# Performance work log

Measured on AMD Instinct MI355X. Metric: run time of the kernel, lower is better.

Reference implementation:

```python
import jax, jax.numpy as jnp
import numpy as np

B, S = 2, 2048
DIM, NH = 2048, 16
QLR, KVLR = 768, 512
NOPE, ROPE, VDIM = 128, 64, 128
IH, IHD, ITOPK = 16, 128, 512
NEG = -1e9


def _rope_half(x, cos, sin):
    # non-interleaved rotary (pairs (x_i, x_{i+d/2})); x: [b,s,h,d], cos/sin: [s,d//2]
    d2 = x.shape[-1] // 2
    x1, x2 = x[..., :d2], x[..., d2:]
    c = cos[None, :, None, :]
    s = sin[None, :, None, :]
    return jnp.concatenate([x1 * c - x2 * s, x1 * s + x2 * c], axis=-1)


def _rmsnorm(x, w, eps=1e-6):
    var = jnp.mean(x * x, axis=-1, keepdims=True)
    return w * x * jax.lax.rsqrt(var + eps)


def _layernorm(x, w, b, eps=1e-6):
    m = jnp.mean(x, axis=-1, keepdims=True)
    v = jnp.mean((x - m) ** 2, axis=-1, keepdims=True)
    return (x - m) * jax.lax.rsqrt(v + eps) * w + b


def setup_inputs() -> dict:
    key = jax.random.key(0)
    ks = jax.random.split(key, 10)

    def w(k, shape):
        return jax.random.normal(k, shape, jnp.float32) * 0.02

    x = jax.random.normal(ks[0], (B, S, DIM), jnp.float32)
    inv_freq = 1.0 / (10000.0 ** (jnp.arange(0, ROPE, 2, dtype=jnp.float32) / ROPE))
    ang = jnp.arange(S, dtype=jnp.float32)[:, None] * inv_freq[None, :]  # [S, ROPE//2]
    causal = jnp.triu(jnp.ones((S, S), dtype=bool), k=1)
    mask = jnp.where(causal, NEG, 0.0).astype(jnp.float32)
    return {
        "x": x,
        "freqs_cos": jnp.cos(ang),
        "freqs_sin": jnp.sin(ang),
        "mask": mask,
        "wq_a": w(ks[1], (QLR, DIM)),
        "q_norm_w": jnp.ones((QLR,), jnp.float32),
        "wq_b": w(ks[2], (NH * (NOPE + ROPE), QLR)),
        "wkv_a": w(ks[3], (KVLR + ROPE, DIM)),
        "kv_norm_w": jnp.ones((KVLR,), jnp.float32),
        "wkv_b": w(ks[4], (NH * (NOPE + VDIM), KVLR)),
        "wo": w(ks[5], (DIM, NH * VDIM)),
        "idx_wq_b": w(ks[6], (IH * IHD, QLR)),
        "idx_wk": w(ks[7], (IHD, DIM)),
        "idx_k_norm_w": jnp.ones((IHD,), jnp.float32),
        "idx_k_norm_b": jnp.zeros((IHD,), jnp.float32),
        "idx_weights_proj": w(ks[8], (IH, DIM)),
        "start_pos": 0,
    }


def _indexer(x, qr, freqs_cos, freqs_sin, mask,
             idx_wq_b, idx_wk, idx_k_norm_w, idx_k_norm_b, idx_weights_proj):
    b, s, _ = x.shape
    q = (qr @ idx_wq_b.T).reshape(b, s, IH, IHD)
    q_pe, q_nope = q[..., :ROPE], q[..., ROPE:]  # rope part FIRST in indexer
    q = jnp.concatenate([_rope_half(q_pe, freqs_cos, freqs_sin), q_nope], axis=-1)
    k = _layernorm(x @ idx_wk.T, idx_k_norm_w, idx_k_norm_b)  # [b,s,IHD]
    k_pe, k_nope = k[..., :ROPE], k[..., ROPE:]
    k_pe = _rope_half(k_pe[:, :, None, :], freqs_cos, freqs_sin)[:, :, 0, :]
    k = jnp.concatenate([k_pe, k_nope], axis=-1)
    # weights_proj(x) * n_heads**-0.5 * softmax_scale(= head_dim**-0.5)
    weights = (x @ idx_weights_proj.T) * (IH ** -0.5) * (IHD ** -0.5)  # [b,s,IH]
    logits = jax.nn.relu(jnp.einsum('bshd,btd->bsth', q, k))
    index_score = jnp.einsum('bsth,bsh->bst', logits, weights) + mask[None]
    _, topk = jax.lax.top_k(index_score, ITOPK)
    return topk  # [b,s,ITOPK] int32


def reference(x, freqs_cos, freqs_sin, mask, wq_a, q_norm_w, wq_b, wkv_a, kv_norm_w,
              wkv_b, wo, idx_wq_b, idx_wk, idx_k_norm_w, idx_k_norm_b,
              idx_weights_proj, start_pos):
    b, s, _ = x.shape
    qr = _rmsnorm(x @ wq_a.T, q_norm_w)  # shared low-rank query latent [b,s,QLR]
    q = (qr @ wq_b.T).reshape(b, s, NH, NOPE + ROPE)
    q_nope, q_pe = q[..., :NOPE], q[..., NOPE:]  # nope part first in MLA
    q_pe = _rope_half(q_pe, freqs_cos, freqs_sin)
    kv = x @ wkv_a.T  # [b,s,KVLR+ROPE]
    kv, k_pe = kv[..., :KVLR], kv[..., KVLR:]
    k_pe = _rope_half(k_pe[:, :, None, :], freqs_cos, freqs_sin)[:, :, 0, :]  # [b,t,ROPE]
    kv = _rmsnorm(kv, kv_norm_w)  # latent kv cache (prefill: full sequence) [b,t,KVLR]
    wkv_b3 = wkv_b.reshape(NH, NOPE + VDIM, KVLR)
    # absorb k up-projection into q (weight absorption trick)
    q_abs = jnp.einsum('bshd,hdc->bshc', q_nope, wkv_b3[:, :NOPE])
    scale = (NOPE + ROPE) ** -0.5
    scores = (jnp.einsum('bshc,btc->bsht', q_abs, kv)
              + jnp.einsum('bshr,btr->bsht', q_pe, k_pe)) * scale
    topk = _indexer(x, qr, freqs_cos, freqs_sin, mask,
                    idx_wq_b, idx_wk, idx_k_norm_w, idx_k_norm_b, idx_weights_proj)
    bi = jnp.arange(b)[:, None, None]
    si = jnp.arange(s)[None, :, None]
    sel = jnp.zeros((b, s, s), dtype=bool).at[bi, si, topk].set(True)
    index_mask = jnp.where(sel, 0.0, NEG) + mask[None]  # [b,s,t]
    scores = scores + index_mask[:, :, None, :]
    p = jax.nn.softmax(scores, axis=-1)
    o = jnp.einsum('bsht,btc->bshc', p, kv)
    o = jnp.einsum('bshc,hdc->bshd', o, wkv_b3[:, NOPE:])  # v up-projection
    return o.reshape(b, s, NH * VDIM) @ wo.T
```

## Files before the change

### kernel.cpp

```cpp
#include <hip/hip_runtime.h>

typedef short bf16x8 __attribute__((ext_vector_type(8)));
typedef _Float16 f16x8 __attribute__((ext_vector_type(8)));
typedef float f32x4 __attribute__((ext_vector_type(4)));
typedef _Float16 f16;
typedef unsigned short u16;
typedef unsigned int u32;

#define DEVFN static __device__ __forceinline__

DEVFN u16 f2bf(float f) {
  u32 u = __builtin_bit_cast(u32, f);
  return (u16)((u + 0x7FFFu + ((u >> 16) & 1u)) >> 16);
}

DEVFN void glds16(const void* g, void* l) {
  __builtin_amdgcn_global_load_lds((const __attribute__((address_space(1))) void*)g,
                                   (__attribute__((address_space(3))) void*)l, 16, 0, 0);
}

DEVFN void wsplit(f16* oh, f16* ol, long o, float v) {
  f16 hh = (f16)v;
  oh[o] = hh;
  ol[o] = (f16)((v - (float)hh) * 2048.0f);
}

DEVFN long idxq_off(int row, int h, int c) {
  return ((((long)(row >> 4) * 16 + h) * 4 + (c >> 5)) * 4 + ((c >> 3) & 3)) * 128
         + (long)(row & 15) * 8 + (c & 7);
}

__global__ __launch_bounds__(256) void k_cvt_bf16(const float* __restrict__ in, u16* __restrict__ out, long n) {
  long i = ((long)blockIdx.x * 256 + threadIdx.x) * 4;
  if (i < n) {
    float4 v = *(const float4*)(in + i);
    out[i] = f2bf(v.x); out[i + 1] = f2bf(v.y); out[i + 2] = f2bf(v.z); out[i + 3] = f2bf(v.w);
  }
}

__global__ __launch_bounds__(256) void k_split(const float* __restrict__ in, f16* __restrict__ oh, f16* __restrict__ ol, long n) {
  long i = ((long)blockIdx.x * 256 + threadIdx.x) * 4;
  if (i < n) {
    float4 v = *(const float4*)(in + i);
    float a[4] = {v.x, v.y, v.z, v.w};
    #pragma unroll
    for (int k = 0; k < 4; ++k) {
      f16 hh = (f16)a[k];
      oh[i + k] = hh;
      ol[i + k] = (f16)((a[k] - (float)hh) * 2048.0f);
    }
  }
}

__global__ __launch_bounds__(256) void k_cvt_split_x(const float* __restrict__ in, u16* __restrict__ ob,
    f16* __restrict__ oh, f16* __restrict__ ol, long n) {
  long i = ((long)blockIdx.x * 256 + threadIdx.x) * 4;
  if (i < n) {
    float4 v = *(const float4*)(in + i);
    float a[4] = {v.x, v.y, v.z, v.w};
    #pragma unroll
    for (int k = 0; k < 4; ++k) {
      ob[i + k] = f2bf(a[k]);
      f16 hh = (f16)a[k];
      oh[i + k] = hh;
      ol[i + k] = (f16)((a[k] - (float)hh) * 2048.0f);
    }
  }
}

__global__ __launch_bounds__(256) void k_cvt_wkvb(const float* __restrict__ wkvb, u16* __restrict__ full_b, u16* __restrict__ nope_t) {
  long i = (long)blockIdx.x * 256 + threadIdx.x;
  if (i >= 2097152) return;
  float v = wkvb[i];
  u16 bv = f2bf(v);
  full_b[i] = bv;
  long row = i >> 9;
  int c = (int)(i & 511);
  int h = (int)(row >> 8);
  int d = (int)(row & 255);
  if (d < 128) nope_t[(long)h * 65536 + (long)c * 128 + d] = bv;
}

__global__ __launch_bounds__(256) void k_gemm_bt(
    const u16* __restrict__ A, const u16* __restrict__ B, void* __restrict__ Cout,
    int N, int K, long lda, long ldb, long ldc, long sA, long sB, long sC, int outBf16) {
  A += (long)blockIdx.z * sA;
  B += (long)blockIdx.z * sB;
  const long m0 = (long)blockIdx.y * 128;
  const long n0 = (long)blockIdx.x * 128;
  __shared__ __align__(16) u16 As[128 * 32];
  __shared__ __align__(16) u16 Bs[128 * 32];
  const int tid = threadIdx.x;
  const int lane = tid & 63, wid = tid >> 6;
  const int g = lane >> 4, l16 = lane & 15;
  const int srow = tid >> 2;
  const int scol = (tid & 3) * 8;
  const int wm = wid >> 1, wn = wid & 1;
  f32x4 acc[4][4];
  #pragma unroll
  for (int m = 0; m < 4; ++m)
    #pragma unroll
    for (int n = 0; n < 4; ++n) acc[m][n] = (f32x4){0.f, 0.f, 0.f, 0.f};
  for (int k0 = 0; k0 < K; k0 += 32) {
    long rb0 = n0 + srow; if (rb0 >= N) rb0 = 0;
    long rb1 = n0 + 64 + srow; if (rb1 >= N) rb1 = 0;
    glds16(A + (m0 + srow) * lda + k0 + scol, As + (size_t)wid * 512);
    glds16(A + (m0 + 64 + srow) * lda + k0 + scol, As + 2048 + (size_t)wid * 512);
    glds16(B + rb0 * ldb + k0 + scol, Bs + (size_t)wid * 512);
    glds16(B + rb1 * ldb + k0 + scol, Bs + 2048 + (size_t)wid * 512);
    __syncthreads();
    bf16x8 af[4], bfv[4];
    #pragma unroll
    for (int m = 0; m < 4; ++m) af[m] = *(const bf16x8*)(As + (wm * 64 + m * 16 + l16) * 32 + g * 8);
    #pragma unroll
    for (int n = 0; n < 4; ++n) bfv[n] = *(const bf16x8*)(Bs + (wn * 64 + n * 16 + l16) * 32 + g * 8);
    #pragma unroll
    for (int m = 0; m < 4; ++m)
      #pragma unroll
      for (int n = 0; n < 4; ++n)
        acc[m][n] = __builtin_amdgcn_mfma_f32_16x16x32_bf16(af[m], bfv[n], acc[m][n], 0, 0, 0);
    __syncthreads();
  }
  const long cz = (long)blockIdx.z * sC;
  if (outBf16) {
    u16* C = (u16*)Cout;
    #pragma unroll
    for (int m = 0; m < 4; ++m) {
      const long row = m0 + wm * 64 + m * 16 + g * 4;
      #pragma unroll
      for (int n = 0; n < 4; ++n) {
        const long col = n0 + wn * 64 + n * 16 + l16;
        if (col < N) {
          #pragma unroll
          for (int r = 0; r < 4; ++r) C[cz + (row + r) * ldc + col] = f2bf(acc[m][n][r]);
        }
      }
    }
  } else {
    float* C = (float*)Cout;
    #pragma unroll
    for (int m = 0; m < 4; ++m) {
      const long row = m0 + wm * 64 + m * 16 + g * 4;
      #pragma unroll
      for (int n = 0; n < 4; ++n) {
        const long col = n0 + wn * 64 + n * 16 + l16;
        if (col < N) {
          #pragma unroll
          for (int r = 0; r < 4; ++r) C[cz + (row + r) * ldc + col] = acc[m][n][r];
        }
      }
    }
  }
}

__global__ __launch_bounds__(256) void k_gemm_f16pair(
    const f16* __restrict__ Ah, const f16* __restrict__ Al,
    const f16* __restrict__ Bh, const f16* __restrict__ Bl,
    float* __restrict__ C, int N, int K, long lda, long ldb, long ldc) {
  const long m0 = (long)blockIdx.y * 128;
  const long n0 = (long)blockIdx.x * 128;
  __shared__ __align__(16) f16 AhS[4096], AlS[4096], BhS[4096], BlS[4096];
  const int tid = threadIdx.x;
  const int lane = tid & 63, wid = tid >> 6;
  const int g = lane >> 4, l16 = lane & 15;
  const int srow = tid >> 2;
  const int scol = (tid & 3) * 8;
  const int wm = wid >> 1, wn = wid & 1;
  f32x4 a0[4][4], a1[4][4];
  #pragma unroll
  for (int m = 0; m < 4; ++m)
    #pragma unroll
    for (int n = 0; n < 4; ++n) { a0[m][n] = (f32x4){0.f,0.f,0.f,0.f}; a1[m][n] = (f32x4){0.f,0.f,0.f,0.f}; }
  for (int k0 = 0; k0 < K; k0 += 32) {
    long rb0 = n0 + srow; if (rb0 >= N) rb0 = 0;
    long rb1 = n0 + 64 + srow; if (rb1 >= N) rb1 = 0;
    glds16(Ah + (m0 + srow) * lda + k0 + scol, AhS + (size_t)wid * 512);
    glds16(Ah + (m0 + 64 + srow) * lda + k0 + scol, AhS + 2048 + (size_t)wid * 512);
    glds16(Al + (m0 + srow) * lda + k0 + scol, AlS + (size_t)wid * 512);
    glds16(Al + (m0 + 64 + srow) * lda + k0 + scol, AlS + 2048 + (size_t)wid * 512);
    glds16(Bh + rb0 * ldb + k0 + scol, BhS + (size_t)wid * 512);
    glds16(Bh + rb1 * ldb + k0 + scol, BhS + 2048 + (size_t)wid * 512);
    glds16(Bl + rb0 * ldb + k0 + scol, BlS + (size_t)wid * 512);
    glds16(Bl + rb1 * ldb + k0 + scol, BlS + 2048 + (size_t)wid * 512);
    __syncthreads();
    f16x8 ah[4], al[4];
    #pragma unroll
    for (int m = 0; m < 4; ++m) {
      ah[m] = *(const f16x8*)(AhS + (wm * 64 + m * 16 + l16) * 32 + g * 8);
      al[m] = *(const f16x8*)(AlS + (wm * 64 + m * 16 + l16) * 32 + g * 8);
    }
    #pragma unroll
    for (int n = 0; n < 4; ++n) {
      f16x8 bh = *(const f16x8*)(BhS + (wn * 64 + n * 16 + l16) * 32 + g * 8);
      f16x8 bl = *(const f16x8*)(BlS + (wn * 64 + n * 16 + l16) * 32 + g * 8);
      #pragma unroll
      for (int m = 0; m < 4; ++m) {
        a0[m][n] = __builtin_amdgcn_mfma_f32_16x16x32_f16(ah[m], bh, a0[m][n], 0, 0, 0);
        a1[m][n] = __builtin_amdgcn_mfma_f32_16x16x32_f16(ah[m], bl, a1[m][n], 0, 0, 0);
        a1[m][n] = __builtin_amdgcn_mfma_f32_16x16x32_f16(al[m], bh, a1[m][n], 0, 0, 0);
      }
    }
    __syncthreads();
  }
  #pragma unroll
  for (int m = 0; m < 4; ++m) {
    const long row = m0 + wm * 64 + m * 16 + g * 4;
    #pragma unroll
    for (int n = 0; n < 4; ++n) {
      const long col = n0 + wn * 64 + n * 16 + l16;
      if (col < N) {
        #pragma unroll
        for (int r = 0; r < 4; ++r)
          C[(row + r) * ldc + col] = a0[m][n][r] + a1[m][n][r] * 4.8828125e-4f;
      }
    }
  }
}

__global__ __launch_bounds__(256) void k_rms_qr(float* __restrict__ qr, const float* __restrict__ w,
    f16* __restrict__ qh, f16* __restrict__ ql, u16* __restrict__ qb) {
  const int row = blockIdx.x, tid = threadIdx.x;
  float v[3];
  float ss = 0.f;
  #pragma unroll
  for (int i = 0; i < 3; ++i) { v[i] = qr[(long)row * 768 + tid + i * 256]; ss += v[i] * v[i]; }
  #pragma unroll
  for (int m = 1; m < 64; m <<= 1) ss += __shfl_xor(ss, m, 64);
  __shared__ float wsum[4];
  if ((tid & 63) == 0) wsum[tid >> 6] = ss;
  __syncthreads();
  float tot = wsum[0] + wsum[1] + wsum[2] + wsum[3];
  float gsc = 1.0f / sqrtf(tot * (1.0f / 768.0f) + 1e-6f);
  #pragma unroll
  for (int i = 0; i < 3; ++i) {
    long o = (long)row * 768 + tid + i * 256;
    float y = v[i] * gsc * w[tid + i * 256];
    qr[o] = y;
    f16 hh = (f16)y;
    qh[o] = hh;
    ql[o] = (f16)((y - (float)hh) * 2048.0f);
    qb[o] = f2bf(y);
  }
}

__global__ __launch_bounds__(256) void k_kvpost(const float* __restrict__ kvraw, const float* __restrict__ w,
    const float* __restrict__ cosb, const float* __restrict__ sinb,
    u16* __restrict__ kvc, u16* __restrict__ kpe) {
  const int row = blockIdx.x, tid = threadIdx.x;
  const int s = row & 2047;
  float v0 = kvraw[(long)row * 576 + tid];
  float v1 = kvraw[(long)row * 576 + 256 + tid];
  float ss = v0 * v0 + v1 * v1;
  #pragma unroll
  for (int m = 1; m < 64; m <<= 1) ss += __shfl_xor(ss, m, 64);
  __shared__ float wsum[4];
  if ((tid & 63) == 0) wsum[tid >> 6] = ss;
  __syncthreads();
  float tot = wsum[0] + wsum[1] + wsum[2] + wsum[3];
  float gsc = 1.0f / sqrtf(tot * (1.0f / 512.0f) + 1e-6f);
  kvc[(long)row * 512 + tid] = f2bf(v0 * gsc * w[tid]);
  kvc[(long)row * 512 + 256 + tid] = f2bf(v1 * gsc * w[256 + tid]);
  if (tid < 32) {
    float x1 = kvraw[(long)row * 576 + 512 + tid];
    float x2 = kvraw[(long)row * 576 + 544 + tid];
    float c = cosb[s * 32 + tid], sn = sinb[s * 32 + tid];
    kpe[(long)row * 64 + tid] = f2bf(x1 * c - x2 * sn);
    kpe[(long)row * 64 + 32 + tid] = f2bf(x1 * sn + x2 * c);
  }
}

__global__ __launch_bounds__(256) void k_qpost(const float* __restrict__ q,
    const float* __restrict__ cosb, const float* __restrict__ sinb,
    u16* __restrict__ qn, u16* __restrict__ qpe) {
  const int row = blockIdx.x, tid = threadIdx.x;
  const int s = row & 2047;
  const long qb = (long)row * 3072;
  #pragma unroll
  for (int i = 0; i < 8; ++i) {
    int idx = tid + i * 256;
    int h = idx >> 7, d = idx & 127;
    qn[(long)row * 2048 + idx] = f2bf(q[qb + h * 192 + d]);
  }
  #pragma unroll
  for (int i = 0; i < 2; ++i) {
    int p = tid + i * 256;
    int h = p >> 5, e = p & 31;
    float x1 = q[qb + h * 192 + 128 + e];
    float x2 = q[qb + h * 192 + 160 + e];
    float c = cosb[s * 32 + e], sn = sinb[s * 32 + e];
    qpe[(long)row * 1024 + h * 64 + e] = f2bf(x1 * c - x2 * sn);
    qpe[(long)row * 1024 + h * 64 + 32 + e] = f2bf(x1 * sn + x2 * c);
  }
}

__global__ __launch_bounds__(256) void k_idxqpost(const float* __restrict__ iq,
    const float* __restrict__ cosb, const float* __restrict__ sinb,
    f16* __restrict__ oh, f16* __restrict__ ol) {
  const int row = blockIdx.x, tid = threadIdx.x;
  const int s = row & 2047;
  const long ib = (long)row * 2048;
  #pragma unroll
  for (int i = 0; i < 2; ++i) {
    int p = tid + i * 256;
    int h = p >> 5, e = p & 31;
    float x1 = iq[ib + h * 128 + e], x2 = iq[ib + h * 128 + 32 + e];
    float c = cosb[s * 32 + e], sn = sinb[s * 32 + e];
    wsplit(oh, ol, idxq_off(row, h, e), x1 * c - x2 * sn);
    wsplit(oh, ol, idxq_off(row, h, e + 32), x1 * sn + x2 * c);
  }
  #pragma unroll
  for (int i = 0; i < 4; ++i) {
    int idx = tid + i * 256;
    int h = idx >> 6, e2 = idx & 63;
    int c = 64 + e2;
    wsplit(oh, ol, idxq_off(row, h, c), iq[ib + h * 128 + c]);
  }
}

__global__ __launch_bounds__(128) void k_idxkpost(const float* __restrict__ ik,
    const float* __restrict__ w, const float* __restrict__ bb,
    const float* __restrict__ cosb, const float* __restrict__ sinb,
    f16* __restrict__ oh, f16* __restrict__ ol) {
  const int row = blockIdx.x, tid = threadIdx.x;
  const int s = row & 2047;
  float v = ik[(long)row * 128 + tid];
  float sum = v;
  #pragma unroll
  for (int m = 1; m < 64; m <<= 1) sum += __shfl_xor(sum, m, 64);
  __shared__ float r0[2], r1[2];
  __shared__ float ybuf[128];
  if ((tid & 63) == 0) r0[tid >> 6] = sum;
  __syncthreads();
  float mean = (r0[0] + r0[1]) * (1.0f / 128.0f);
  float d = v - mean;
  float s2 = d * d;
  #pragma unroll
  for (int m = 1; m < 64; m <<= 1) s2 += __shfl_xor(s2, m, 64);
  if ((tid & 63) == 0) r1[tid >> 6] = s2;
  __syncthreads();
  float var = (r1[0] + r1[1]) * (1.0f / 128.0f);
  float y = d * (1.0f / sqrtf(var + 1e-6f)) * w[tid] + bb[tid];
  ybuf[tid] = y;
  __syncthreads();
  float outv = y;
  if (tid < 64) {
    int e = tid & 31;
    float x1 = ybuf[e], x2 = ybuf[32 + e];
    float c = cosb[s * 32 + e], sn = sinb[s * 32 + e];
    outv = (tid < 32) ? (x1 * c - x2 * sn) : (x1 * sn + x2 * c);
  }
  int csw = tid ^ ((row & 7) << 3);
  long o = (long)row * 128 + csw;
  f16 hh = (f16)outv;
  oh[o] = hh;
  ol[o] = (f16)((outv - (float)hh) * 2048.0f);
}

__global__ __launch_bounds__(256) void k_wproj(const float* __restrict__ x,
    const float* __restrict__ proj, float* __restrict__ out) {
  const int row = blockIdx.x, tid = threadIdx.x;
  __shared__ float xr[2048];
  #pragma unroll
  for (int i = 0; i < 8; ++i) xr[tid + i * 256] = x[(long)row * 2048 + tid + i * 256];
  __syncthreads();
  int h = tid >> 4, seg = tid & 15;
  float acc = 0.f;
  for (int k = 0; k < 128; ++k) acc += xr[seg * 128 + k] * proj[h * 2048 + seg * 128 + k];
  #pragma unroll
  for (int m = 1; m < 16; m <<= 1) acc += __shfl_xor(acc, m, 64);
  if (seg == 0) out[(long)row * 16 + h] = acc * 0.25f * 0.08838834764831843f;
}

__global__ __launch_bounds__(256) void k_iscore(
    const f16* __restrict__ Ah, const f16* __restrict__ Al,
    const f16* __restrict__ Bh, const f16* __restrict__ Bl,
    const float* __restrict__ wts, float* __restrict__ out) {
  const int b = blockIdx.z;
  const int s0 = blockIdx.y * 64, t0 = blockIdx.x * 128;
  if (t0 > s0 + 63) return;
  __shared__ __align__(16) f16 BhS[128 * 128];
  __shared__ __align__(16) f16 BlS[128 * 128];
  const int tid = threadIdx.x;
  const int lane = tid & 63, wid = tid >> 6;
  const int g = lane >> 4, l16 = lane & 15;
  const long brow = ((long)b * 2048 + t0) * 128;
  #pragma unroll
  for (int c = 0; c < 8; ++c) {
    int row = c * 16 + (tid >> 4);
    int col = (tid & 15) * 8;
    glds16(Bh + brow + (long)row * 128 + col, BhS + (size_t)c * 2048 + (size_t)wid * 512);
    glds16(Bl + brow + (long)row * 128 + col, BlS + (size_t)c * 2048 + (size_t)wid * 512);
  }
  __syncthreads();
  const int ws_ = wid >> 1, wt = wid & 1;
  f32x4 sc[2][4];
  #pragma unroll
  for (int m = 0; m < 2; ++m)
    #pragma unroll
    for (int n = 0; n < 4; ++n) sc[m][n] = (f32x4){0.f, 0.f, 0.f, 0.f};
  for (int h = 0; h < 16; ++h) {
    f16x8 ah[2][4], al[2][4];
    #pragma unroll
    for (int m = 0; m < 2; ++m) {
      int rt = (b * 2048 + s0 + ws_ * 32 + m * 16) >> 4;
      #pragma unroll
      for (int kc = 0; kc < 4; ++kc) {
        long o = ((((long)rt * 16 + h) * 4 + kc) * 4 + g) * 128 + l16 * 8;
        ah[m][kc] = *(const f16x8*)(Ah + o);
        al[m][kc] = *(const f16x8*)(Al + o);
      }
    }
    f32x4 l0[2][4], l1[2][4];
    #pragma unroll
    for (int m = 0; m < 2; ++m)
      #pragma unroll
      for (int n = 0; n < 4; ++n) { l0[m][n] = (f32x4){0.f,0.f,0.f,0.f}; l1[m][n] = (f32x4){0.f,0.f,0.f,0.f}; }
    #pragma unroll
    for (int kc = 0; kc < 4; ++kc) {
      #pragma unroll
      for (int n = 0; n < 4; ++n) {
        int row = wt * 64 + n * 16 + l16;
        int ecol = (kc * 32 + g * 8) ^ ((row & 7) * 8);
        f16x8 bh = *(const f16x8*)(BhS + row * 128 + ecol);
        f16x8 bl = *(const f16x8*)(BlS + row * 128 + ecol);
        #pragma unroll
        for (int m = 0; m < 2; ++m) {
          l0[m][n] = __builtin_amdgcn_mfma_f32_16x16x32_f16(ah[m][kc], bh, l0[m][n], 0, 0, 0);
          l1[m][n] = __builtin_amdgcn_mfma_f32_16x16x32_f16(ah[m][kc], bl, l1[m][n], 0, 0, 0);
          l1[m][n] = __builtin_amdgcn_mfma_f32_16x16x32_f16(al[m][kc], bh, l1[m][n], 0, 0, 0);
        }
      }
    }
    #pragma unroll
    for (int m = 0; m < 2; ++m) {
      #pragma unroll
      for (int r = 0; r < 4; ++r) {
        float wv = wts[((long)b * 2048 + s0 + ws_ * 32 + m * 16 + g * 4 + r) * 16 + h];
        #pragma unroll
        for (int n = 0; n < 4; ++n) {
          float lg = l0[m][n][r] + l1[m][n][r] * 4.8828125e-4f;
          if (lg > 0.f) sc[m][n][r] += lg * wv;
        }
      }
    }
  }
  #pragma unroll
  for (int m = 0; m < 2; ++m) {
    #pragma unroll
    for (int n = 0; n < 4; ++n) {
      int tcol = t0 + wt * 64 + n * 16 + l16;
      #pragma unroll
      for (int r = 0; r < 4; ++r) {
        int srow = s0 + ws_ * 32 + m * 16 + g * 4 + r;
        out[((long)b * 2048 + srow) * 2048 + tcol] = sc[m][n][r];
      }
    }
  }
}

__global__ __launch_bounds__(256) void k_topk(const float* __restrict__ scores, int* __restrict__ sel) {
  const int bs = blockIdx.x;
  const int s = bs & 2047;
  const int n = s + 1;
  const int tid = threadIdx.x;
  int* out = sel + (long)bs * 512;
  if (n <= 512) {
    for (int i = tid; i < 512; i += 256) out[i] = (i < n) ? i : -1;
    return;
  }
  const float* sr = scores + (long)bs * 2048;
  __shared__ u32 hist[256];
  __shared__ u32 sh_prefix;
  __shared__ int sh_R, sh_cnt, sh_tiebase;
  __shared__ int sh_wcnt[4];
  if (tid == 0) { sh_prefix = 0; sh_R = 512; }
  for (int pass = 0; pass < 4; ++pass) {
    int shift = 24 - pass * 8;
    for (int i = tid; i < 256; i += 256) hist[i] = 0;
    __syncthreads();
    u32 pfx = sh_prefix;
    int R = sh_R;
    for (int t = tid; t < n; t += 256) {
      u32 u = __builtin_bit_cast(u32, sr[t]);
      u = (u & 0x80000000u) ? ~u : (u | 0x80000000u);
      bool ok = (pass == 0) || ((u >> (shift + 8)) == (pfx >> (shift + 8)));
      if (ok) atomicAdd(&hist[(u >> shift) & 255], 1u);
    }
    __syncthreads();
    if (tid == 0) {
      int cum = 0, v = 255;
      for (; v >= 0; --v) {
        int c = (int)hist[v];
        if (cum + c >= R) break;
        cum += c;
      }
      sh_prefix = pfx | ((u32)v << shift);
      sh_R = R - cum;
    }
    __syncthreads();
  }
  const u32 thr = sh_prefix;
  const int R = sh_R;
  if (tid == 0) { sh_cnt = 0; sh_tiebase = 0; }
  __syncthreads();
  for (int t = tid; t < n; t += 256) {
    u32 u = __builtin_bit_cast(u32, sr[t]);
    u = (u & 0x80000000u) ? ~u : (u | 0x80000000u);
    if (u > thr) out[atomicAdd(&sh_cnt, 1)] = t;
  }
  __syncthreads();
  const int base = sh_cnt;
  for (int c0 = 0; c0 < n; c0 += 256) {
    int t = c0 + tid;
    bool f = false;
    if (t < n) {
      u32 u = __builtin_bit_cast(u32, sr[t]);
      u = (u & 0x80000000u) ? ~u : (u | 0x80000000u);
      f = (u == thr);
    }
    unsigned long long mk = __ballot(f);
    int lane = tid & 63, w = tid >> 6;
    int rank = __popcll(mk & ((1ull << lane) - 1ull));
    if (lane == 0) sh_wcnt[w] = __popcll(mk);
    __syncthreads();
    int wbase = 0;
    for (int i = 0; i < w; ++i) wbase += sh_wcnt[i];
    int tb = sh_tiebase;
    if (f) {
      int pos = tb + wbase + rank;
      if (pos < R) out[base + pos] = t;
    }
    __syncthreads();
    if (tid == 0) sh_tiebase = tb + sh_wcnt[0] + sh_wcnt[1] + sh_wcnt[2] + sh_wcnt[3];
    __syncthreads();
  }
}

#define KSTR 584
__global__ __launch_bounds__(256) void k_attn(
    const int* __restrict__ sel, const u16* __restrict__ qabs, const u16* __restrict__ qpe,
    const u16* __restrict__ kvc, const u16* __restrict__ kpe, u16* __restrict__ oc) {
  const int bs = blockIdx.x;
  const int b = bs >> 11;
  const int tid = threadIdx.x;
  const int lane = tid & 63, wid = tid >> 6;
  const int g = lane >> 4, l16 = lane & 15;
  __shared__ __align__(16) u16 K_lds[32 * KSTR];
  __shared__ float S_lds[2 * 16 * 36];
  __shared__ __align__(16) u16 P_lds[16 * 40];
  __shared__ int t_tile[32];
  __shared__ float m_lds[16], l_lds[16], f_lds[16];
  if (tid < 16) { m_lds[tid] = -3e38f; l_lds[tid] = 0.f; }
  const int half = wid >> 1, jhalf = wid & 1;
  const int kcb = half * 9;
  bf16x8 qf[9];
  #pragma unroll
  for (int i = 0; i < 9; ++i) {
    int kc = kcb + i;
    if (kc < 16) qf[i] = *(const bf16x8*)(qabs + ((long)bs * 16 + l16) * 512 + kc * 32 + g * 8);
    else qf[i] = *(const bf16x8*)(qpe + ((long)bs * 16 + l16) * 64 + (kc - 16) * 32 + g * 8);
  }
  f32x4 oacc[8];
  #pragma unroll
  for (int cf = 0; cf < 8; ++cf) oacc[cf] = (f32x4){0.f, 0.f, 0.f, 0.f};
  __syncthreads();
  for (int jt = 0; jt < 16; ++jt) {
    #pragma unroll
    for (int it = 0; it < 2; ++it) {
      int cid = it * 256 + tid;
      if (cid < 288) {
        int jr = cid / 9, part = cid % 9;
        int t = sel[(long)bs * 512 + jt * 32 + jr];
        if (part == 0) t_tile[jr] = t;
        int te = t < 0 ? 0 : t;
        const u16* src = (part < 8) ? (kvc + ((long)(b * 2048 + te)) * 512 + part * 64)
                                    : (kpe + ((long)(b * 2048 + te)) * 64);
        const uint4* s4 = (const uint4*)src;
        const int swz = ((jr >> 3) & 3) << 4;
        if (part < 8) {
          #pragma unroll
          for (int i = 0; i < 8; ++i) {
            int cs = (part * 64 + i * 8) ^ swz;
            *(uint4*)&K_lds[jr * KSTR + cs] = s4[i];
          }
        } else {
          #pragma unroll
          for (int i = 0; i < 8; ++i)
            *(uint4*)&K_lds[jr * KSTR + 512 + i * 8] = s4[i];
        }
      }
    }
    __syncthreads();
    const int key = jhalf * 16 + l16;
    const int kswz = ((key >> 3) & 3) << 4;
    f32x4 sacc = (f32x4){0.f, 0.f, 0.f, 0.f};
    #pragma unroll
    for (int i = 0; i < 9; ++i) {
      int kc = kcb + i;
      bf16x8 bfr;
      if (kc < 16) {
        int cs = (kc * 32 + g * 8) ^ kswz;
        bfr = *(const bf16x8*)&K_lds[key * KSTR + cs];
      } else {
        bfr = *(const bf16x8*)&K_lds[key * KSTR + kc * 32 + g * 8];
      }
      sacc = __builtin_amdgcn_mfma_f32_16x16x32_bf16(qf[i], bfr, sacc, 0, 0, 0);
    }
    int tj = t_tile[key];
    #pragma unroll
    for (int r = 0; r < 4; ++r) {
      int h = g * 4 + r;
      S_lds[half * 576 + h * 36 + key] = (tj < 0) ? -1e30f : sacc[r] * 0.07216878364870322f;
    }
    __syncthreads();
    {
      int h = tid >> 4, q16 = tid & 15;
      float vs[2];
      float mx = -3e38f;
      #pragma unroll
      for (int k = 0; k < 2; ++k) {
        int j = q16 + k * 16;
        vs[k] = S_lds[h * 36 + j] + S_lds[576 + h * 36 + j];
        mx = fmaxf(mx, vs[k]);
      }
      #pragma unroll
      for (int m = 1; m < 16; m <<= 1) mx = fmaxf(mx, __shfl_xor(mx, m, 64));
      float m_old = m_lds[h];
      float m_new = fmaxf(m_old, mx);
      float ps = 0.f;
      #pragma unroll
      for (int k = 0; k < 2; ++k) {
        float p = __expf(vs[k] - m_new);
        ps += p;
        P_lds[h * 40 + q16 + k * 16] = f2bf(p);
      }
      #pragma unroll
      for (int m = 1; m < 16; m <<= 1) ps += __shfl_xor(ps, m, 64);
      if (q16 == 0) {
        float f = __expf(m_old - m_new);
        f_lds[h] = f;
        m_lds[h] = m_new;
        l_lds[h] = l_lds[h] * f + ps;
      }
    }
    __syncthreads();
    float fr[4];
    #pragma unroll
    for (int r = 0; r < 4; ++r) fr[r] = f_lds[g * 4 + r];
    #pragma unroll
    for (int cf = 0; cf < 8; ++cf)
      #pragma unroll
      for (int r = 0; r < 4; ++r) oacc[cf][r] *= fr[r];
    bf16x8 pa = *(const bf16x8*)&P_lds[l16 * 40 + g * 8];
    #pragma unroll
    for (int cf = 0; cf < 8; ++cf) {
      int colv = (wid * 128 + cf * 16 + l16) ^ (g << 4);
      bf16x8 vb;
      #pragma unroll
      for (int e = 0; e < 8; ++e) vb[e] = (short)K_lds[(g * 8 + e) * KSTR + colv];
      oacc[cf] = __builtin_amdgcn_mfma_f32_16x16x32_bf16(pa, vb, oacc[cf], 0, 0, 0);
    }
    __syncthreads();
  }
  float li[4];
  #pragma unroll
  for (int r = 0; r < 4; ++r) li[r] = 1.0f / l_lds[g * 4 + r];
  #pragma unroll
  for (int cf = 0; cf < 8; ++cf) {
    int col = wid * 128 + cf * 16 + l16;
    #pragma unroll
    for (int r = 0; r < 4; ++r) {
      int h = g * 4 + r;
      oc[((long)bs * 16 + h) * 512 + col] = f2bf(oacc[cf][r] * li[r]);
    }
  }
}

extern "C" void kernel_launch(void* const* d_in, const int* in_sizes, int n_in,
                              void* d_out, int out_size, void* d_ws, size_t ws_size,
                              hipStream_t stream) {
  const float* x = (const float*)d_in[0];
  const float* fcos = (const float*)d_in[1];
  const float* fsin = (const float*)d_in[2];
  const float* wq_a = (const float*)d_in[4];
  const float* q_norm_w = (const float*)d_in[5];
  const float* wq_b = (const float*)d_in[6];
  const float* wkv_a = (const float*)d_in[7];
  const float* kv_norm_w = (const float*)d_in[8];
  const float* wkv_b = (const float*)d_in[9];
  const float* wo = (const float*)d_in[10];
  const float* idx_wq_b = (const float*)d_in[11];
  const float* idx_wk = (const float*)d_in[12];
  const float* iknw = (const float*)d_in[13];
  const float* iknb = (const float*)d_in[14];
  const float* iwp = (const float*)d_in[15];

  size_t off = 0;
  char* wsb = (char*)d_ws;
  auto alloc = [&](size_t bytes) -> char* {
    char* p = wsb + off;
    off += (bytes + 255) & ~(size_t)255;
    return p;
  };
  u16* x_b16  = (u16*)alloc(16777216);
  f16* xh     = (f16*)alloc(16777216);
  f16* xl     = (f16*)alloc(16777216);
  f16* wqa_h  = (f16*)alloc(3145728);
  f16* wqa_l  = (f16*)alloc(3145728);
  float* qr   = (float*)alloc(12582912);
  f16* qr_h   = (f16*)alloc(6291456);
  f16* qr_l   = (f16*)alloc(6291456);
  u16* qr_b   = (u16*)alloc(6291456);
  u16* wqb_b  = (u16*)alloc(4718592);
  char* QBIG  = alloc(50331648);
  u16* qn_b   = (u16*)alloc(16777216);
  u16* qpe_b  = (u16*)alloc(8388608);
  u16* wkva_b = (u16*)alloc(2359296);
  float* kvraw= (float*)alloc(9437184);
  u16* kvc_b  = (u16*)alloc(4194304);
  u16* kpe_b  = (u16*)alloc(524288);
  u16* wkvb_b = (u16*)alloc(4194304);
  u16* wkvbnt = (u16*)alloc(2097152);
  u16* wo_b   = (u16*)alloc(8388608);
  f16* iwqb_h = (f16*)alloc(3145728);
  f16* iwqb_l = (f16*)alloc(3145728);
  f16* idxq_h = (f16*)alloc(16777216);
  f16* idxq_l = (f16*)alloc(16777216);
  f16* iwk_h  = (f16*)alloc(524288);
  f16* iwk_l  = (f16*)alloc(524288);
  float* idxk_f = (float*)alloc(2097152);
  f16* idxk_h = (f16*)alloc(1048576);
  f16* idxk_l = (f16*)alloc(1048576);
  float* idxw = (float*)alloc(262144);
  int* sel    = (int*)alloc(8388608);
  u16* q_abs  = (u16*)xh;
  float* q_f32 = (float*)QBIG;
  float* idxq_f32 = (float*)QBIG;
  float* scores = (float*)QBIG;
  u16* o_c    = (u16*)QBIG;
  u16* o_d    = (u16*)idxq_h;

  k_cvt_split_x<<<8192, 256, 0, stream>>>(x, x_b16, xh, xl, 8388608L);
  k_split<<<1536, 256, 0, stream>>>(wq_a, wqa_h, wqa_l, 1572864L);
  k_cvt_bf16<<<2304, 256, 0, stream>>>(wq_b, wqb_b, 2359296L);
  k_cvt_bf16<<<1152, 256, 0, stream>>>(wkv_a, wkva_b, 1179648L);
  k_cvt_wkvb<<<8192, 256, 0, stream>>>(wkv_b, wkvb_b, wkvbnt);
  k_cvt_bf16<<<4096, 256, 0, stream>>>(wo, wo_b, 4194304L);
  k_split<<<1536, 256, 0, stream>>>(idx_wq_b, iwqb_h, iwqb_l, 1572864L);
  k_split<<<256, 256, 0, stream>>>(idx_wk, iwk_h, iwk_l, 262144L);

  k_gemm_f16pair<<<dim3(6, 32, 1), 256, 0, stream>>>(xh, xl, wqa_h, wqa_l, qr, 768, 2048, 2048, 2048, 768);
  k_rms_qr<<<4096, 256, 0, stream>>>(qr, q_norm_w, qr_h, qr_l, qr_b);

  k_gemm_bt<<<dim3(24, 32, 1), 256, 0, stream>>>(qr_b, wqb_b, QBIG, 3072, 768, 768, 768, 3072, 0, 0, 0, 0);
  k_qpost<<<4096, 256, 0, stream>>>(q_f32, fcos, fsin, qn_b, qpe_b);

  k_gemm_bt<<<dim3(5, 32, 1), 256, 0, stream>>>(x_b16, wkva_b, kvraw, 576, 2048, 2048, 2048, 576, 0, 0, 0, 0);
  k_kvpost<<<4096, 256, 0, stream>>>(kvraw, kv_norm_w, fcos, fsin, kvc_b, kpe_b);

  k_gemm_f16pair<<<dim3(16, 32, 1), 256, 0, stream>>>(qr_h, qr_l, iwqb_h, iwqb_l, idxq_f32, 2048, 768, 768, 768, 2048);
  k_idxqpost<<<4096, 256, 0, stream>>>(idxq_f32, fcos, fsin, idxq_h, idxq_l);
  k_gemm_f16pair<<<dim3(1, 32, 1), 256, 0, stream>>>(xh, xl, iwk_h, iwk_l, idxk_f, 128, 2048, 2048, 2048, 128);
  k_idxkpost<<<4096, 128, 0, stream>>>(idxk_f, iknw, iknb, fcos, fsin, idxk_h, idxk_l);
  k_wproj<<<4096, 256, 0, stream>>>(x, iwp, idxw);

  k_gemm_bt<<<dim3(4, 32, 16), 256, 0, stream>>>(qn_b, wkvbnt, q_abs, 512, 128, 2048, 128, 8192, 128, 65536, 512, 1);

  k_iscore<<<dim3(16, 32, 2), 256, 0, stream>>>(idxq_h, idxq_l, idxk_h, idxk_l, idxw, scores);
  k_topk<<<4096, 256, 0, stream>>>(scores, sel);

  k_attn<<<4096, 256, 0, stream>>>(sel, q_abs, qpe_b, kvc_b, kpe_b, o_c);

  k_gemm_bt<<<dim3(1, 32, 16), 256, 0, stream>>>(o_c, wkvb_b + 65536, o_d, 128, 512, 8192, 512, 2048, 512, 131072, 128, 1);
  k_gemm_bt<<<dim3(16, 32, 1), 256, 0, stream>>>(o_d, wo_b, d_out, 2048, 2048, 2048, 2048, 2048, 0, 0, 0, 0);
}
```

Measured before the change: 1.532 ms.

## Gather KV via async global-to-LDS loads with transposed LDS reads and prefetch

Replaces the per-thread register-staged gather of selected KV rows into a padded, swizzled LDS tile with direct global_load_lds 16-byte transfers into a new blocked layout. The V operand for the PV MFMA is now read with ds_read_b64_tr_b16 transposed reads instead of eight scalar LDS loads per fragment. The next tile's gather is issued after the softmax barrier so it overlaps with the PV MFMAs. The risk is that the single LDS buffer is overwritten while still in use: the V fragments are read into registers early, but correct ordering depends on the barrier placement and on the async load counters.

```diff
diff --git a/kernel.cpp b/kernel.cpp
--- a/kernel.cpp
+++ b/kernel.cpp
@@ -1,6 +1,7 @@
 #include <hip/hip_runtime.h>
 
 typedef short bf16x8 __attribute__((ext_vector_type(8)));
+typedef short s16x4 __attribute__((ext_vector_type(4)));
 typedef _Float16 f16x8 __attribute__((ext_vector_type(8)));
 typedef float f32x4 __attribute__((ext_vector_type(4)));
 typedef _Float16 f16;
@@ -17,6 +18,22 @@
 DEVFN void glds16(const void* g, void* l) {
   __builtin_amdgcn_global_load_lds((const __attribute__((address_space(1))) void*)g,
                                    (__attribute__((address_space(3))) void*)l, 16, 0, 0);
+}
+
+DEVFN u32 lds_u32(const void* p) {
+  return (u32)(size_t)(const __attribute__((address_space(3))) void*)p;
+}
+
+DEVFN s16x4 ds_tr16(u32 addr) {
+  s16x4 d;
+  asm volatile("ds_read_b64_tr_b16 %0, %1" : "=v"(d) : "v"(addr));
+  return d;
+}
+
+DEVFN bf16x8 combine8(s16x4 a, s16x4 b) {
+  union { s16x4 h[2]; bf16x8 v; } u;
+  u.h[0] = a; u.h[1] = b;
+  return u.v;
 }
 
 DEVFN void wsplit(f16* oh, f16* ol, long o, float v) {
@@ -536,7 +553,6 @@
   }
 }
 
-#define KSTR 584
 __global__ __launch_bounds__(256) void k_attn(
     const int* __restrict__ sel, const u16* __restrict__ qabs, const u16* __restrict__ qpe,
     const u16* __restrict__ kvc, const u16* __restrict__ kpe, u16* __restrict__ oc) {
@@ -545,7 +561,7 @@
   const int tid = threadIdx.x;
   const int lane = tid & 63, wid = tid >> 6;
   const int g = lane >> 4, l16 = lane & 15;
-  __shared__ __align__(16) u16 K_lds[32 * KSTR];
+  __shared__ __align__(16) u16 V_lds[36 * 512];
   __shared__ float S_lds[2 * 16 * 36];
   __shared__ __align__(16) u16 P_lds[16 * 40];
   __shared__ int t_tile[32];
@@ -560,51 +576,46 @@
     if (kc < 16) qf[i] = *(const bf16x8*)(qabs + ((long)bs * 16 + l16) * 512 + kc * 32 + g * 8);
     else qf[i] = *(const bf16x8*)(qpe + ((long)bs * 16 + l16) * 64 + (kc - 16) * 32 + g * 8);
   }
+  const int gk = ((lane >> 3) & 3) * 8 + (lane >> 5) * 4 + ((lane >> 1) & 3);
+  const int ch = lane & 1;
+  const int key = jhalf * 16 + l16;
+  const int keyoff = ((key >> 2) & 1) * 256 + (key >> 3) * 64 + (key & 3) * 16;
   f32x4 oacc[8];
   #pragma unroll
   for (int cf = 0; cf < 8; ++cf) oacc[cf] = (f32x4){0.f, 0.f, 0.f, 0.f};
-  __syncthreads();
+
+  {
+    int t = sel[(long)bs * 512 + gk];
+    int te = t < 0 ? 0 : t;
+    if (wid == 0 && ch == 0) t_tile[gk] = t;
+    const u16* srcv = kvc + ((long)(b * 2048 + te)) * 512 + ch * 8;
+    const u16* srcp = kpe + ((long)(b * 2048 + te)) * 64 + ch * 8;
+    #pragma unroll
+    for (int q = 0; q < 9; ++q) {
+      int cblk = wid * 9 + q;
+      const u16* src = (cblk < 32) ? (srcv + cblk * 16) : (srcp + (cblk - 32) * 16);
+      glds16(src, (char*)V_lds + cblk * 1024);
+    }
+  }
+  __syncthreads();
+
   for (int jt = 0; jt < 16; ++jt) {
-    #pragma unroll
-    for (int it = 0; it < 2; ++it) {
-      int cid = it * 256 + tid;
-      if (cid < 288) {
-        int jr = cid / 9, part = cid % 9;
-        int t = sel[(long)bs * 512 + jt * 32 + jr];
-        if (part == 0) t_tile[jr] = t;
-        int te = t < 0 ? 0 : t;
-        const u16* src = (part < 8) ? (kvc + ((long)(b * 2048 + te)) * 512 + part * 64)
-                                    : (kpe + ((long)(b * 2048 + te)) * 64);
-        const uint4* s4 = (const uint4*)src;
-        const int swz = ((jr >> 3) & 3) << 4;
-        if (part < 8) {
-          #pragma unroll
-          for (int i = 0; i < 8; ++i) {
-            int cs = (part * 64 + i * 8) ^ swz;
-            *(uint4*)&K_lds[jr * KSTR + cs] = s4[i];
-          }
-        } else {
-          #pragma unroll
-          for (int i = 0; i < 8; ++i)
-            *(uint4*)&K_lds[jr * KSTR + 512 + i * 8] = s4[i];
-        }
-      }
-    }
-    __syncthreads();
-    const int key = jhalf * 16 + l16;
-    const int kswz = ((key >> 3) & 3) << 4;
     f32x4 sacc = (f32x4){0.f, 0.f, 0.f, 0.f};
     #pragma unroll
     for (int i = 0; i < 9; ++i) {
       int kc = kcb + i;
-      bf16x8 bfr;
-      if (kc < 16) {
-        int cs = (kc * 32 + g * 8) ^ kswz;
-        bfr = *(const bf16x8*)&K_lds[key * KSTR + cs];
-      } else {
-        bfr = *(const bf16x8*)&K_lds[key * KSTR + kc * 32 + g * 8];
-      }
+      int addr = (kc * 2 + (g >> 1)) * 512 + keyoff + (g & 1) * 8;
+      bf16x8 bfr = *(const bf16x8*)(V_lds + addr);
       sacc = __builtin_amdgcn_mfma_f32_16x16x32_bf16(qf[i], bfr, sacc, 0, 0, 0);
+    }
+    s16x4 tv0[8], tv1[8];
+    {
+      u32 trb = lds_u32(V_lds) + (u32)(wid * 8192 + lane * 8);
+      #pragma unroll
+      for (int cf = 0; cf < 8; ++cf) {
+        tv0[cf] = ds_tr16(trb + cf * 1024);
+        tv1[cf] = ds_tr16(trb + cf * 1024 + 512);
+      }
     }
     int tj = t_tile[key];
     #pragma unroll
@@ -644,20 +655,28 @@
       }
     }
     __syncthreads();
+    if (jt < 15) {
+      int t = sel[(long)bs * 512 + (jt + 1) * 32 + gk];
+      int te = t < 0 ? 0 : t;
+      if (wid == 0 && ch == 0) t_tile[gk] = t;
+      const u16* srcv = kvc + ((long)(b * 2048 + te)) * 512 + ch * 8;
+      const u16* srcp = kpe + ((long)(b * 2048 + te)) * 64 + ch * 8;
+      #pragma unroll
+      for (int q = 0; q < 9; ++q) {
+        int cblk = wid * 9 + q;
+        const u16* src = (cblk < 32) ? (srcv + cblk * 16) : (srcp + (cblk - 32) * 16);
+        glds16(src, (char*)V_lds + cblk * 1024);
+      }
+    }
     float fr[4];
     #pragma unroll
     for (int r = 0; r < 4; ++r) fr[r] = f_lds[g * 4 + r];
-    #pragma unroll
-    for (int cf = 0; cf < 8; ++cf)
+    bf16x8 pa = *(const bf16x8*)&P_lds[l16 * 40 + g * 8];
+    #pragma unroll
+    for (int cf = 0; cf < 8; ++cf) {
       #pragma unroll
       for (int r = 0; r < 4; ++r) oacc[cf][r] *= fr[r];
-    bf16x8 pa = *(const bf16x8*)&P_lds[l16 * 40 + g * 8];
-    #pragma unroll
-    for (int cf = 0; cf < 8; ++cf) {
-      int colv = (wid * 128 + cf * 16 + l16) ^ (g << 4);
-      bf16x8 vb;
-      #pragma unroll
-      for (int e = 0; e < 8; ++e) vb[e] = (short)K_lds[(g * 8 + e) * KSTR + colv];
+      bf16x8 vb = combine8(tv0[cf], tv1[cf]);
       oacc[cf] = __builtin_amdgcn_mfma_f32_16x16x32_bf16(pa, vb, oacc[cf], 0, 0, 0);
     }
     __syncthreads();
```

New measurement: 1.296 ms. 1.18x faster.
